# Kernel tuning notes

Measured on AMD Instinct MI355X. Metric: run time of the kernel, lower is better.

## Reference

```python
import jax, jax.numpy as jnp
import numpy as np

V, D, S, L_LAYERS, T_MAX = 32000, 512, 256, 4, 2048
DFF = ((int(8 / 3 * D)) + 7) // 8 * 8  # 1368
EPS = 1e-5


def _ln(x, w, b):
    mu = jnp.mean(x, axis=-1, keepdims=True)
    var = jnp.mean((x - mu) ** 2, axis=-1, keepdims=True)
    return (x - mu) * jax.lax.rsqrt(var + EPS) * w + b


def _next_pow2(n):
    m = 1
    while m < n:
        m *= 2
    return m


def setup_inputs() -> dict:
    key = jax.random.key(0)
    ks = jax.random.split(key, 20)
    B, T = 2, 2048
    inp = {
        "x": jax.random.randint(ks[0], (B, T), 0, V),
        "emb": jax.random.normal(ks[1], (V, D), jnp.float32) * 0.02,
        "pos": jax.random.normal(ks[2], (T_MAX, D), jnp.float32) * 0.02,
        "log_lambda": jax.random.uniform(ks[3], (L_LAYERS, S), jnp.float32, 2.94, 4.6),
        "Bw": jax.random.normal(ks[4], (L_LAYERS, S, D), jnp.float32) * 0.04,
        "Cw": jax.random.normal(ks[5], (L_LAYERS, D, S), jnp.float32) * 0.04,
        "Dp": jnp.ones((L_LAYERS, D), jnp.float32),
        "n1w": jnp.ones((L_LAYERS, D), jnp.float32),
        "n1b": jnp.zeros((L_LAYERS, D), jnp.float32),
        "n2w": jnp.ones((L_LAYERS, D), jnp.float32),
        "n2b": jnp.zeros((L_LAYERS, D), jnp.float32),
        "w1": jax.random.normal(ks[6], (L_LAYERS, DFF, D), jnp.float32) * 0.04,
        "w2": jax.random.normal(ks[7], (L_LAYERS, DFF, D), jnp.float32) * 0.04,
        "w3": jax.random.normal(ks[8], (L_LAYERS, D, DFF), jnp.float32) * 0.03,
        "now": jnp.ones((D,), jnp.float32),
        "nob": jnp.zeros((D,), jnp.float32),
        "headW": jax.random.normal(ks[9], (V, D), jnp.float32) * 0.02,
        "headb": jnp.zeros((V,), jnp.float32),
    }
    return inp


def _ssm(u, log_lam, Bw, Cw, Dp):
    # u: [B, T, D]; causal per-channel conv k_j[t] = lambda_j^t via FFT
    B_, T_, _ = u.shape
    fft_len = _next_pow2(2 * T_)
    Bu = jnp.einsum("btd,sd->bts", u, Bw)  # [B, T, S]
    lam = jax.nn.sigmoid(log_lam)  # [S]
    t = jnp.arange(T_, dtype=lam.dtype)
    kernel = lam[None, :] ** t[:, None]  # [T, S]
    Kh = jnp.fft.rfft(kernel, n=fft_len, axis=0)  # [F, S]
    Buh = jnp.fft.rfft(Bu, n=fft_len, axis=1)  # [B, F, S]
    h = jnp.fft.irfft(Kh[None] * Buh, n=fft_len, axis=1)[:, :T_, :]
    return jnp.einsum("bts,ds->btd", h, Cw) + Dp * u


def _swiglu(x, w1, w2, w3):
    return jnp.einsum("btf,df->btd", jax.nn.silu(jnp.einsum("btd,fd->btf", x, w1)) * jnp.einsum("btd,fd->btf", x, w2), w3)


def reference(x, emb, pos, log_lambda, Bw, Cw, Dp, n1w, n1b, n2w, n2b, w1, w2, w3, now, nob, headW, headb):
    B_, T_ = x.shape
    h = emb[x] + pos[jnp.arange(T_)][None]  # [B, T, D]
    for l in range(L_LAYERS):
        h = h + _ssm(_ln(h, n1w[l], n1b[l]), log_lambda[l], Bw[l], Cw[l], Dp[l])
        h = h + _swiglu(_ln(h, n2w[l], n2b[l]), w1[l], w2[l], w3[l])
    h = _ln(h, now, nob)
    return jnp.einsum("btd,vd->btv", h, headW) + headb
```

## Files before the change

### kernel.cpp

```cpp
#include <hip/hip_runtime.h>
#include <hip/hip_bf16.h>

#define TT 2048
#define BT 4096
#define DD 512
#define SS 256
#define VV 32000
#define LL 4
#define DFF_ 1368
#define DFFP 1408

typedef __attribute__((ext_vector_type(8))) short s16x8;
typedef __attribute__((ext_vector_type(4))) float f32x4;

static __device__ __forceinline__ unsigned short f2bf(float x) {
  __hip_bfloat16 t = __float2bfloat16(x);
  return __builtin_bit_cast(unsigned short, t);
}
static __device__ __forceinline__ float bf2f(unsigned short u) {
  __hip_bfloat16 t = __builtin_bit_cast(__hip_bfloat16, u);
  return __bfloat162float(t);
}

__global__ void cast_kernel(const float* __restrict__ s, unsigned short* __restrict__ d, long n) {
  long i = (long)blockIdx.x * 256 + threadIdx.x;
  if (i < n) d[i] = f2bf(s[i]);
}

__global__ void cast_pad_rows_kernel(const float* __restrict__ s, unsigned short* __restrict__ d,
                                     int R0, int R1, int C) {
  long i = (long)blockIdx.x * 256 + threadIdx.x;
  long n = (long)LL * R1 * C;
  if (i >= n) return;
  int c = (int)(i % C);
  long t2 = i / C;
  int r = (int)(t2 % R1);
  int l = (int)(t2 / R1);
  float v = (r < R0) ? s[((long)l * R0 + r) * C + c] : 0.f;
  d[i] = f2bf(v);
}

__global__ void cast_pad_cols_kernel(const float* __restrict__ s, unsigned short* __restrict__ d,
                                     int R, int C0, int C1) {
  long i = (long)blockIdx.x * 256 + threadIdx.x;
  long n = (long)LL * R * C1;
  if (i >= n) return;
  int c = (int)(i % C1);
  long t2 = i / C1;
  int r = (int)(t2 % R);
  int l = (int)(t2 / R);
  float v = (c < C0) ? s[((long)l * R + r) * C0 + c] : 0.f;
  d[i] = f2bf(v);
}

__global__ void embed_kernel(const int* __restrict__ x, const float* __restrict__ emb,
                             const float* __restrict__ pos, float* __restrict__ h) {
  int row = blockIdx.x;
  int t = row & (TT - 1);
  int tok = x[row];
  const float4* e = (const float4*)(emb + (long)tok * DD);
  const float4* p = (const float4*)(pos + (long)t * DD);
  float4* o = (float4*)(h + (long)row * DD);
  int i = threadIdx.x;
  float4 a = e[i], b = p[i];
  float4 r;
  r.x = a.x + b.x; r.y = a.y + b.y; r.z = a.z + b.z; r.w = a.w + b.w;
  o[i] = r;
}

template <int WF32>
__global__ __launch_bounds__(256) void ln_kernel(const float* __restrict__ h, const float* __restrict__ w,
                                                 const float* __restrict__ b, float* __restrict__ uf,
                                                 unsigned short* __restrict__ ub) {
  int row = blockIdx.x * 4 + (threadIdx.x >> 6);
  int lane = threadIdx.x & 63;
  const float* hr = h + (long)row * DD + lane * 8;
  float x[8];
  *(float4*)(x) = *(const float4*)(hr);
  *(float4*)(x + 4) = *(const float4*)(hr + 4);
  float s = 0.f;
#pragma unroll
  for (int i = 0; i < 8; ++i) s += x[i];
#pragma unroll
  for (int off = 32; off; off >>= 1) s += __shfl_xor(s, off);
  float mu = s * (1.f / 512.f);
  float q = 0.f;
#pragma unroll
  for (int i = 0; i < 8; ++i) { x[i] -= mu; q += x[i] * x[i]; }
#pragma unroll
  for (int off = 32; off; off >>= 1) q += __shfl_xor(q, off);
  float rstd = rsqrtf(q * (1.f / 512.f) + 1e-5f);
  float wv[8], bv[8];
  *(float4*)(wv) = *(const float4*)(w + lane * 8);
  *(float4*)(wv + 4) = *(const float4*)(w + lane * 8 + 4);
  *(float4*)(bv) = *(const float4*)(b + lane * 8);
  *(float4*)(bv + 4) = *(const float4*)(b + lane * 8 + 4);
  float y[8];
  s16x8 pk;
#pragma unroll
  for (int i = 0; i < 8; ++i) {
    y[i] = x[i] * rstd * wv[i] + bv[i];
    pk[i] = (short)f2bf(y[i]);
  }
  if (WF32) {
    float* up = uf + (long)row * DD + lane * 8;
    *(float4*)(up) = *(const float4*)(y);
    *(float4*)(up + 4) = *(const float4*)(y + 4);
  }
  *(s16x8*)(ub + (long)row * DD + lane * 8) = pk;
}

__global__ void scan1_kernel(const float* __restrict__ Bu, const float* __restrict__ ll,
                             float* __restrict__ E) {
  int s = threadIdx.x;
  int c = blockIdx.x & 63;
  int b = blockIdx.x >> 6;
  float lam = 1.f / (1.f + __expf(-ll[s]));
  const float* p = Bu + ((long)b * TT + c * 32) * SS + s;
  float hacc = 0.f;
#pragma unroll
  for (int i = 0; i < 32; ++i) hacc = fmaf(lam, hacc, p[i * SS]);
  E[((long)b * 64 + c) * SS + s] = hacc;
}

__global__ void scan2_kernel(const float* __restrict__ E, const float* __restrict__ ll,
                             float* __restrict__ Hin) {
  int tid = threadIdx.x;
  int s = tid & 255;
  int b = tid >> 8;
  float lam = 1.f / (1.f + __expf(-ll[s]));
  float l2 = lam * lam, l4 = l2 * l2, l8 = l4 * l4, l16 = l8 * l8, l32 = l16 * l16;
  float carry = 0.f;
  for (int c = 0; c < 64; ++c) {
    long idx = ((long)b * 64 + c) * SS + s;
    Hin[idx] = carry;
    carry = fmaf(l32, carry, E[idx]);
  }
}

__global__ void scan3_kernel(const float* __restrict__ Bu, const float* __restrict__ ll,
                             const float* __restrict__ Hin, unsigned short* __restrict__ hst) {
  int s = threadIdx.x;
  int c = blockIdx.x & 63;
  int b = blockIdx.x >> 6;
  float lam = 1.f / (1.f + __expf(-ll[s]));
  const float* p = Bu + ((long)b * TT + c * 32) * SS + s;
  unsigned short* o = hst + ((long)b * TT + c * 32) * SS + s;
  float hacc = Hin[((long)b * 64 + c) * SS + s];
#pragma unroll
  for (int i = 0; i < 32; ++i) {
    hacc = fmaf(lam, hacc, p[i * SS]);
    o[i * SS] = f2bf(hacc);
  }
}

template <int EPI>
__global__ __launch_bounds__(256) void gemm_bt(const unsigned short* __restrict__ A,
                                               const unsigned short* __restrict__ W, int mtiles, int N,
                                               int K, float* __restrict__ of,
                                               unsigned short* __restrict__ ob,
                                               const float* __restrict__ e0,
                                               const float* __restrict__ e1,
                                               const unsigned short* __restrict__ e2) {
  __shared__ unsigned short As[128 * 32];
  __shared__ unsigned short Ws[128 * 32];
  int bm = blockIdx.x % mtiles;
  int bn = blockIdx.x / mtiles;
  int t = threadIdx.x, lane = t & 63, wv = t >> 6;
  int wm = (wv >> 1) * 64, wn = (wv & 1) * 64;
  f32x4 acc[4][4] = {};
  const unsigned short* Ab = A + (long)bm * 128 * K;
  const unsigned short* Wb = W + (long)bn * 128 * K;
  int r0 = t >> 2;
  int eo = (t & 3) * 8;
  int r16 = lane & 15, kg = (lane >> 4) * 8;

  for (int kt = 0; kt < K; kt += 32) {
    s16x8 a0 = *(const s16x8*)(Ab + (long)r0 * K + kt + eo);
    s16x8 a1 = *(const s16x8*)(Ab + (long)(r0 + 64) * K + kt + eo);
    s16x8 w0 = *(const s16x8*)(Wb + (long)r0 * K + kt + eo);
    s16x8 w1 = *(const s16x8*)(Wb + (long)(r0 + 64) * K + kt + eo);
    __syncthreads();
    *(s16x8*)(As + t * 8) = a0;
    *(s16x8*)(As + t * 8 + 2048) = a1;
    *(s16x8*)(Ws + t * 8) = w0;
    *(s16x8*)(Ws + t * 8 + 2048) = w1;
    __syncthreads();
    s16x8 af[4], wf[4];
#pragma unroll
    for (int f = 0; f < 4; ++f) af[f] = *(const s16x8*)(As + (wm + f * 16 + r16) * 32 + kg);
#pragma unroll
    for (int f = 0; f < 4; ++f) wf[f] = *(const s16x8*)(Ws + (wn + f * 16 + r16) * 32 + kg);
#pragma unroll
    for (int fm = 0; fm < 4; ++fm)
#pragma unroll
      for (int fn = 0; fn < 4; ++fn)
        acc[fm][fn] = __builtin_amdgcn_mfma_f32_16x16x32_bf16(af[fm], wf[fn], acc[fm][fn], 0, 0, 0);
  }

  long mb = (long)bm * 128 + wm + ((lane >> 4) * 4);
  int nb = bn * 128 + wn + (lane & 15);
#pragma unroll
  for (int fm = 0; fm < 4; ++fm) {
#pragma unroll
    for (int j = 0; j < 4; ++j) {
      long m = mb + fm * 16 + j;
#pragma unroll
      for (int fn = 0; fn < 4; ++fn) {
        int n = nb + fn * 16;
        long idx = m * N + n;
        float v = acc[fm][fn][j];
        if constexpr (EPI == 0) {
          of[idx] = v;
        } else if constexpr (EPI == 1) {
          of[idx] += v + e0[n] * e1[idx];
        } else if constexpr (EPI == 2) {
          float sg = v / (1.f + __expf(-v));
          ob[idx] = f2bf(sg);
        } else if constexpr (EPI == 3) {
          ob[idx] = f2bf(bf2f(e2[idx]) * v);
        } else if constexpr (EPI == 4) {
          of[idx] += v;
        } else {
          of[idx] = v + e0[n];
        }
      }
    }
  }
}

extern "C" void kernel_launch(void* const* d_in, const int* in_sizes, int n_in, void* d_out,
                              int out_size, void* d_ws, size_t ws_size, hipStream_t stream) {
  const int* x = (const int*)d_in[0];
  const float* emb = (const float*)d_in[1];
  const float* pos = (const float*)d_in[2];
  const float* loglam = (const float*)d_in[3];
  const float* Bw = (const float*)d_in[4];
  const float* Cw = (const float*)d_in[5];
  const float* Dp = (const float*)d_in[6];
  const float* n1w = (const float*)d_in[7];
  const float* n1b = (const float*)d_in[8];
  const float* n2w = (const float*)d_in[9];
  const float* n2b = (const float*)d_in[10];
  const float* w1 = (const float*)d_in[11];
  const float* w2 = (const float*)d_in[12];
  const float* w3 = (const float*)d_in[13];
  const float* now_ = (const float*)d_in[14];
  const float* nob = (const float*)d_in[15];
  const float* headW = (const float*)d_in[16];
  const float* headb = (const float*)d_in[17];

  unsigned short* headW_bf = (unsigned short*)d_ws;
  unsigned short* hf_bf = (unsigned short*)((char*)d_ws + (size_t)VV * DD * 2);

  char* ob_ = (char*)d_out;
  float* h = (float*)(ob_ + 0);
  float* u = (float*)(ob_ + 8388608);
  unsigned short* ubf = (unsigned short*)(ob_ + 16777216);
  float* Bu = (float*)(ob_ + 20971520);
  unsigned short* hst = (unsigned short*)(ob_ + 25165824);
  float* E = (float*)(ob_ + 27262976);
  float* Hin = (float*)(ob_ + 27394048);
  unsigned short* s1 = (unsigned short*)(ob_ + 27525120);
  unsigned short* gate = (unsigned short*)(ob_ + 39059456);
  unsigned short* Bw_bf = (unsigned short*)(ob_ + 50593792);
  unsigned short* Cw_bf = (unsigned short*)(ob_ + 51642368);
  unsigned short* w1_bf = (unsigned short*)(ob_ + 52690944);
  unsigned short* w2_bf = (unsigned short*)(ob_ + 58458112);
  unsigned short* w3_bf = (unsigned short*)(ob_ + 64225280);

  cast_kernel<<<2048, 256, 0, stream>>>(Bw, Bw_bf, (long)LL * SS * DD);
  cast_kernel<<<2048, 256, 0, stream>>>(Cw, Cw_bf, (long)LL * DD * SS);
  cast_kernel<<<64000, 256, 0, stream>>>(headW, headW_bf, (long)VV * DD);
  cast_pad_rows_kernel<<<11264, 256, 0, stream>>>(w1, w1_bf, DFF_, DFFP, DD);
  cast_pad_rows_kernel<<<11264, 256, 0, stream>>>(w2, w2_bf, DFF_, DFFP, DD);
  cast_pad_cols_kernel<<<11264, 256, 0, stream>>>(w3, w3_bf, DD, DFF_, DFFP);
  embed_kernel<<<BT, 128, 0, stream>>>(x, emb, pos, h);

  for (int l = 0; l < LL; ++l) {
    ln_kernel<1><<<BT / 4, 256, 0, stream>>>(h, n1w + l * DD, n1b + l * DD, u, ubf);
    gemm_bt<0><<<32 * (SS / 128), 256, 0, stream>>>(ubf, Bw_bf + (long)l * SS * DD, 32, SS, DD, Bu,
                                                    nullptr, nullptr, nullptr, nullptr);
    scan1_kernel<<<128, 256, 0, stream>>>(Bu, loglam + l * SS, E);
    scan2_kernel<<<1, 512, 0, stream>>>(E, loglam + l * SS, Hin);
    scan3_kernel<<<128, 256, 0, stream>>>(Bu, loglam + l * SS, Hin, hst);
    gemm_bt<1><<<32 * (DD / 128), 256, 0, stream>>>(hst, Cw_bf + (long)l * DD * SS, 32, DD, SS, h,
                                                    nullptr, Dp + l * DD, u, nullptr);
    ln_kernel<0><<<BT / 4, 256, 0, stream>>>(h, n2w + l * DD, n2b + l * DD, nullptr, ubf);
    gemm_bt<2><<<32 * (DFFP / 128), 256, 0, stream>>>(ubf, w1_bf + (long)l * DFFP * DD, 32, DFFP, DD,
                                                      nullptr, s1, nullptr, nullptr, nullptr);
    gemm_bt<3><<<32 * (DFFP / 128), 256, 0, stream>>>(ubf, w2_bf + (long)l * DFFP * DD, 32, DFFP, DD,
                                                      nullptr, gate, nullptr, nullptr, s1);
    gemm_bt<4><<<32 * (DD / 128), 256, 0, stream>>>(gate, w3_bf + (long)l * DD * DFFP, 32, DD, DFFP, h,
                                                    nullptr, nullptr, nullptr, nullptr);
  }
  ln_kernel<0><<<BT / 4, 256, 0, stream>>>(h, now_, nob, nullptr, hf_bf);
  gemm_bt<5><<<32 * (VV / 128), 256, 0, stream>>>(hf_bf, headW_bf, 32, VV, DD, (float*)d_out, nullptr,
                                                  headb, nullptr, nullptr);
}
```

Before: 1.323 ms.

## Fuse SwiGLU gate GEMMs with interleaved weights, use direct global-to-LDS loads

The w1 and w2 weights are interleaved row-by-row into one matrix, so a single GEMM computes both projections. The epilogue pairs adjacent columns with a lane shuffle to form silu(a)*b, which removes one GEMM launch and the bf16 intermediate round trip. The GEMM tile loads now use global_load_lds to bypass registers, the weight-cast kernels are vectorised to 8 elements per thread, and scan2 is register-buffered. The direct-to-LDS path relies on the builtin's per-lane address semantics matching the existing LDS layout.

```diff
diff --git a/kernel.cpp b/kernel.cpp
--- a/kernel.cpp
+++ b/kernel.cpp
@@ -22,35 +22,55 @@
   return __bfloat162float(t);
 }
 
-__global__ void cast_kernel(const float* __restrict__ s, unsigned short* __restrict__ d, long n) {
+static __device__ __forceinline__ void gl2lds16(const unsigned short* g, unsigned short* l) {
+  __builtin_amdgcn_global_load_lds(
+      (const __attribute__((address_space(1))) unsigned int*)(g),
+      (__attribute__((address_space(3))) unsigned int*)(l), 16, 0, 0);
+}
+
+__global__ void cast8_kernel(const float* __restrict__ s, unsigned short* __restrict__ d, long n8) {
   long i = (long)blockIdx.x * 256 + threadIdx.x;
-  if (i < n) d[i] = f2bf(s[i]);
-}
-
-__global__ void cast_pad_rows_kernel(const float* __restrict__ s, unsigned short* __restrict__ d,
-                                     int R0, int R1, int C) {
+  if (i >= n8) return;
+  const float* p = s + i * 8;
+  float4 a = *(const float4*)p, b = *(const float4*)(p + 4);
+  s16x8 o;
+  o[0] = (short)f2bf(a.x); o[1] = (short)f2bf(a.y); o[2] = (short)f2bf(a.z); o[3] = (short)f2bf(a.w);
+  o[4] = (short)f2bf(b.x); o[5] = (short)f2bf(b.y); o[6] = (short)f2bf(b.z); o[7] = (short)f2bf(b.w);
+  *(s16x8*)(d + i * 8) = o;
+}
+
+__global__ void cast_ilv8_kernel(const float* __restrict__ w1, const float* __restrict__ w2,
+                                 unsigned short* __restrict__ d) {
   long i = (long)blockIdx.x * 256 + threadIdx.x;
-  long n = (long)LL * R1 * C;
-  if (i >= n) return;
-  int c = (int)(i % C);
-  long t2 = i / C;
-  int r = (int)(t2 % R1);
-  int l = (int)(t2 / R1);
-  float v = (r < R0) ? s[((long)l * R0 + r) * C + c] : 0.f;
-  d[i] = f2bf(v);
-}
-
-__global__ void cast_pad_cols_kernel(const float* __restrict__ s, unsigned short* __restrict__ d,
-                                     int R, int C0, int C1) {
+  if (i >= (long)LL * 2 * DFFP * 64) return;
+  int c8 = (int)(i & 63);
+  long t2 = i >> 6;
+  int r = (int)(t2 % (2 * DFFP));
+  int l = (int)(t2 / (2 * DFFP));
+  int f = r >> 1;
+  s16x8 o = {0, 0, 0, 0, 0, 0, 0, 0};
+  if (f < DFF_) {
+    const float* src = ((r & 1) ? w2 : w1) + ((long)l * DFF_ + f) * DD + c8 * 8;
+    float4 a = *(const float4*)src, b = *(const float4*)(src + 4);
+    o[0] = (short)f2bf(a.x); o[1] = (short)f2bf(a.y); o[2] = (short)f2bf(a.z); o[3] = (short)f2bf(a.w);
+    o[4] = (short)f2bf(b.x); o[5] = (short)f2bf(b.y); o[6] = (short)f2bf(b.z); o[7] = (short)f2bf(b.w);
+  }
+  *(s16x8*)(d + ((long)l * (2 * DFFP) + r) * DD + c8 * 8) = o;
+}
+
+__global__ void cast_padc8_kernel(const float* __restrict__ s, unsigned short* __restrict__ d) {
   long i = (long)blockIdx.x * 256 + threadIdx.x;
-  long n = (long)LL * R * C1;
-  if (i >= n) return;
-  int c = (int)(i % C1);
-  long t2 = i / C1;
-  int r = (int)(t2 % R);
-  int l = (int)(t2 / R);
-  float v = (c < C0) ? s[((long)l * R + r) * C0 + c] : 0.f;
-  d[i] = f2bf(v);
+  if (i >= (long)LL * DD * (DFFP / 8)) return;
+  int g = (int)(i % (DFFP / 8));
+  long row = i / (DFFP / 8);
+  s16x8 o = {0, 0, 0, 0, 0, 0, 0, 0};
+  if (g < DFF_ / 8) {
+    const float* src = s + row * DFF_ + g * 8;
+    float4 a = *(const float4*)src, b = *(const float4*)(src + 4);
+    o[0] = (short)f2bf(a.x); o[1] = (short)f2bf(a.y); o[2] = (short)f2bf(a.z); o[3] = (short)f2bf(a.w);
+    o[4] = (short)f2bf(b.x); o[5] = (short)f2bf(b.y); o[6] = (short)f2bf(b.z); o[7] = (short)f2bf(b.w);
+  }
+  *(s16x8*)(d + row * DFFP + g * 8) = o;
 }
 
 __global__ void embed_kernel(const int* __restrict__ x, const float* __restrict__ emb,
@@ -130,12 +150,20 @@
   int b = tid >> 8;
   float lam = 1.f / (1.f + __expf(-ll[s]));
   float l2 = lam * lam, l4 = l2 * l2, l8 = l4 * l4, l16 = l8 * l8, l32 = l16 * l16;
+  const float* Ep = E + (long)b * 64 * SS + s;
+  float* Hp = Hin + (long)b * 64 * SS + s;
+  float e[64];
+#pragma unroll
+  for (int c = 0; c < 64; ++c) e[c] = Ep[c * SS];
   float carry = 0.f;
+#pragma unroll
   for (int c = 0; c < 64; ++c) {
-    long idx = ((long)b * 64 + c) * SS + s;
-    Hin[idx] = carry;
-    carry = fmaf(l32, carry, E[idx]);
-  }
+    float t = e[c];
+    e[c] = carry;
+    carry = fmaf(l32, carry, t);
+  }
+#pragma unroll
+  for (int c = 0; c < 64; ++c) Hp[c * SS] = e[c];
 }
 
 __global__ void scan3_kernel(const float* __restrict__ Bu, const float* __restrict__ ll,
@@ -160,13 +188,13 @@
                                                int K, float* __restrict__ of,
                                                unsigned short* __restrict__ ob,
                                                const float* __restrict__ e0,
-                                               const float* __restrict__ e1,
-                                               const unsigned short* __restrict__ e2) {
+                                               const float* __restrict__ e1) {
   __shared__ unsigned short As[128 * 32];
   __shared__ unsigned short Ws[128 * 32];
   int bm = blockIdx.x % mtiles;
   int bn = blockIdx.x / mtiles;
-  int t = threadIdx.x, lane = t & 63, wv = t >> 6;
+  int t = threadIdx.x, lane = t & 63;
+  int wv = t >> 6;
   int wm = (wv >> 1) * 64, wn = (wv & 1) * 64;
   f32x4 acc[4][4] = {};
   const unsigned short* Ab = A + (long)bm * 128 * K;
@@ -176,15 +204,11 @@
   int r16 = lane & 15, kg = (lane >> 4) * 8;
 
   for (int kt = 0; kt < K; kt += 32) {
-    s16x8 a0 = *(const s16x8*)(Ab + (long)r0 * K + kt + eo);
-    s16x8 a1 = *(const s16x8*)(Ab + (long)(r0 + 64) * K + kt + eo);
-    s16x8 w0 = *(const s16x8*)(Wb + (long)r0 * K + kt + eo);
-    s16x8 w1 = *(const s16x8*)(Wb + (long)(r0 + 64) * K + kt + eo);
     __syncthreads();
-    *(s16x8*)(As + t * 8) = a0;
-    *(s16x8*)(As + t * 8 + 2048) = a1;
-    *(s16x8*)(Ws + t * 8) = w0;
-    *(s16x8*)(Ws + t * 8 + 2048) = w1;
+    gl2lds16(Ab + (long)r0 * K + kt + eo, As + t * 8);
+    gl2lds16(Ab + (long)(r0 + 64) * K + kt + eo, As + 2048 + t * 8);
+    gl2lds16(Wb + (long)r0 * K + kt + eo, Ws + t * 8);
+    gl2lds16(Wb + (long)(r0 + 64) * K + kt + eo, Ws + 2048 + t * 8);
     __syncthreads();
     s16x8 af[4], wf[4];
 #pragma unroll
@@ -214,15 +238,16 @@
           of[idx] = v;
         } else if constexpr (EPI == 1) {
           of[idx] += v + e0[n] * e1[idx];
-        } else if constexpr (EPI == 2) {
-          float sg = v / (1.f + __expf(-v));
-          ob[idx] = f2bf(sg);
-        } else if constexpr (EPI == 3) {
-          ob[idx] = f2bf(bf2f(e2[idx]) * v);
         } else if constexpr (EPI == 4) {
           of[idx] += v;
-        } else {
+        } else if constexpr (EPI == 5) {
           of[idx] = v + e0[n];
+        } else if constexpr (EPI == 6) {
+          float po = __shfl_xor(v, 1);
+          if ((lane & 1) == 0) {
+            float sg = v / (1.f + __expf(-v));
+            ob[m * (long)(N >> 1) + (n >> 1)] = f2bf(sg * po);
+          }
         }
       }
     }
@@ -261,40 +286,36 @@
   unsigned short* hst = (unsigned short*)(ob_ + 25165824);
   float* E = (float*)(ob_ + 27262976);
   float* Hin = (float*)(ob_ + 27394048);
-  unsigned short* s1 = (unsigned short*)(ob_ + 27525120);
-  unsigned short* gate = (unsigned short*)(ob_ + 39059456);
-  unsigned short* Bw_bf = (unsigned short*)(ob_ + 50593792);
-  unsigned short* Cw_bf = (unsigned short*)(ob_ + 51642368);
-  unsigned short* w1_bf = (unsigned short*)(ob_ + 52690944);
-  unsigned short* w2_bf = (unsigned short*)(ob_ + 58458112);
-  unsigned short* w3_bf = (unsigned short*)(ob_ + 64225280);
-
-  cast_kernel<<<2048, 256, 0, stream>>>(Bw, Bw_bf, (long)LL * SS * DD);
-  cast_kernel<<<2048, 256, 0, stream>>>(Cw, Cw_bf, (long)LL * DD * SS);
-  cast_kernel<<<64000, 256, 0, stream>>>(headW, headW_bf, (long)VV * DD);
-  cast_pad_rows_kernel<<<11264, 256, 0, stream>>>(w1, w1_bf, DFF_, DFFP, DD);
-  cast_pad_rows_kernel<<<11264, 256, 0, stream>>>(w2, w2_bf, DFF_, DFFP, DD);
-  cast_pad_cols_kernel<<<11264, 256, 0, stream>>>(w3, w3_bf, DD, DFF_, DFFP);
+  unsigned short* gate = (unsigned short*)(ob_ + 27525120);
+  unsigned short* Bw_bf = (unsigned short*)(ob_ + 39059456);
+  unsigned short* Cw_bf = (unsigned short*)(ob_ + 40108032);
+  unsigned short* w12_bf = (unsigned short*)(ob_ + 41156608);
+  unsigned short* w3_bf = (unsigned short*)(ob_ + 52690944);
+
+  cast8_kernel<<<1024, 256, 0, stream>>>(Bw, Bw_bf, (long)LL * SS * DD / 8);
+  cast8_kernel<<<1024, 256, 0, stream>>>(Cw, Cw_bf, (long)LL * DD * SS / 8);
+  cast8_kernel<<<8000, 256, 0, stream>>>(headW, headW_bf, (long)VV * DD / 8);
+  cast_ilv8_kernel<<<5632, 256, 0, stream>>>(w1, w2, w12_bf);
+  cast_padc8_kernel<<<1408, 256, 0, stream>>>(w3, w3_bf);
   embed_kernel<<<BT, 128, 0, stream>>>(x, emb, pos, h);
 
   for (int l = 0; l < LL; ++l) {
     ln_kernel<1><<<BT / 4, 256, 0, stream>>>(h, n1w + l * DD, n1b + l * DD, u, ubf);
     gemm_bt<0><<<32 * (SS / 128), 256, 0, stream>>>(ubf, Bw_bf + (long)l * SS * DD, 32, SS, DD, Bu,
-                                                    nullptr, nullptr, nullptr, nullptr);
+                                                    nullptr, nullptr, nullptr);
     scan1_kernel<<<128, 256, 0, stream>>>(Bu, loglam + l * SS, E);
     scan2_kernel<<<1, 512, 0, stream>>>(E, loglam + l * SS, Hin);
     scan3_kernel<<<128, 256, 0, stream>>>(Bu, loglam + l * SS, Hin, hst);
     gemm_bt<1><<<32 * (DD / 128), 256, 0, stream>>>(hst, Cw_bf + (long)l * DD * SS, 32, DD, SS, h,
-                                                    nullptr, Dp + l * DD, u, nullptr);
+                                                    nullptr, Dp + l * DD, u);
     ln_kernel<0><<<BT / 4, 256, 0, stream>>>(h, n2w + l * DD, n2b + l * DD, nullptr, ubf);
-    gemm_bt<2><<<32 * (DFFP / 128), 256, 0, stream>>>(ubf, w1_bf + (long)l * DFFP * DD, 32, DFFP, DD,
-                                                      nullptr, s1, nullptr, nullptr, nullptr);
-    gemm_bt<3><<<32 * (DFFP / 128), 256, 0, stream>>>(ubf, w2_bf + (long)l * DFFP * DD, 32, DFFP, DD,
-                                                      nullptr, gate, nullptr, nullptr, s1);
-    gemm_bt<4><<<32 * (DD / 128), 256, 0, stream>>>(gate, w3_bf + (long)l * DD * DFFP, 32, DD, DFFP, h,
-                                                    nullptr, nullptr, nullptr, nullptr);
+    gemm_bt<6><<<32 * (2 * DFFP / 128), 256, 0, stream>>>(ubf, w12_bf + (long)l * 2 * DFFP * DD, 32,
+                                                          2 * DFFP, DD, nullptr, gate, nullptr,
+                                                          nullptr);
+    gemm_bt<4><<<32 * (DD / 128), 256, 0, stream>>>(gate, w3_bf + (long)l * DD * DFFP, 32, DD, DFFP,
+                                                    h, nullptr, nullptr, nullptr);
   }
   ln_kernel<0><<<BT / 4, 256, 0, stream>>>(h, now_, nob, nullptr, hf_bf);
-  gemm_bt<5><<<32 * (VV / 128), 256, 0, stream>>>(hf_bf, headW_bf, 32, VV, DD, (float*)d_out, nullptr,
-                                                  headb, nullptr, nullptr);
-}
+  gemm_bt<5><<<32 * (VV / 128), 256, 0, stream>>>(hf_bf, headW_bf, 32, VV, DD, (float*)d_out,
+                                                  nullptr, headb, nullptr);
+}
```

Result: faster. 1.249 ms (-5.6%).
